# Kernel tuning notes

Measured on AMD Instinct MI355X. Metric: run time of the kernel, lower is better.

The kernel has to match this reference:

```python
import jax, jax.numpy as jnp
import numpy as np

B, L, E, H = 64, 512, 1024, 1024


def setup_inputs() -> dict:
    key = jax.random.key(0)
    ks = jax.random.split(key, 12)
    u = lambda k, s: jax.random.uniform(k, s, jnp.float32, -0.1, 0.1)
    inp = {
        "inputs": jax.random.normal(ks[0], (B, L, E), jnp.float32),
        "input_m": jax.random.randint(ks[1], (B, L), 0, 2).astype(jnp.int32),
    }
    # torch Linear convention: y = x @ W.T + b; biases init to 0 per init_weights()
    for j, n in enumerate(["f", "i", "o", "c"]):
        inp[f"W{n}x"] = u(ks[2 + j], (H, E))
        inp[f"b{n}x"] = jnp.zeros((H,), jnp.float32)
        inp[f"W{n}m"] = u(ks[6 + j], (H, H))
        inp[f"b{n}m"] = jnp.zeros((H,), jnp.float32)
    return inp


def _lstm(inputs, mask_f, Wfx, bfx, Wix, bix, Wox, box, Wcx, bcx,
          Wfm, bfm, Wim, bim, Wom, bom, Wcm, bcm):
    # Fuse the 4 input projections into one GEMM over all timesteps (same math)
    Wx = jnp.concatenate([Wfx, Wix, Wox, Wcx], axis=0)   # [4H, E]
    bx = jnp.concatenate([bfx, bix, box, bcx], axis=0)   # [4H]
    Wm = jnp.concatenate([Wfm, Wim, Wom, Wcm], axis=0)   # [4H, H]
    bm = jnp.concatenate([bfm, bim, bom, bcm], axis=0)   # [4H]

    xproj = jnp.einsum('ble,ge->blg', inputs, Wx) + bx   # [B, L, 4H]
    xs = jnp.moveaxis(xproj, 1, 0)                       # [L, B, 4H]
    ms = mask_f.T[:, :, None]                            # [L, B, 1]

    h0 = jnp.zeros((inputs.shape[0], Wm.shape[1]), inputs.dtype)
    c0 = jnp.zeros_like(h0)

    def step(carry, xm):
        h, c = carry
        xg, m = xm
        g = xg + h @ Wm.T + bm                           # [B, 4H]
        f, i, o, ct = jnp.split(g, 4, axis=-1)
        f = jax.nn.sigmoid(f)
        i = jax.nn.sigmoid(i)
        o = jax.nn.sigmoid(o)
        ct = jnp.tanh(ct)
        c_new = f * c + i * ct                           # cell always updated (as in source)
        hx = o * jnp.tanh(c_new)
        h_new = hx * m + h * (1.0 - m)                   # mask applies to hidden only
        return (h_new, c_new), h_new

    (h_t, c_t), outs = jax.lax.scan(step, (h0, c0), (xs, ms))
    outputs = jnp.moveaxis(outs, 0, 1)                   # [B, L, H]
    return outputs, h_t, c_t


def reference(inputs, input_m, Wfx, bfx, Wix, bix, Wox, box, Wcx, bcx,
              Wfm, bfm, Wim, bim, Wom, bom, Wcm, bcm):
    mask_f = input_m.astype(inputs.dtype)
    return _lstm(inputs, mask_f, Wfx, bfx, Wix, bix, Wox, box, Wcx, bcx,
                 Wfm, bfm, Wim, bim, Wom, bom, Wcm, bcm)
```

## Files before the change

kernel.cpp:

```cpp
#include <hip/hip_runtime.h>


#define B_   64
#define L_   512
#define E_   1024
#define H_   1024

typedef __attribute__((ext_vector_type(8))) short bf16x8;
typedef __attribute__((ext_vector_type(4))) float f32x4;

#define MFMA16(a, b, c) __builtin_amdgcn_mfma_f32_16x16x32_bf16((a), (b), (c), 0, 0, 0)

__device__ __forceinline__ unsigned short f2b(float f) {
  unsigned int u = __float_as_uint(f);
  u += 0x7fffu + ((u >> 16) & 1u);
  return (unsigned short)(u >> 16);
}

__device__ __forceinline__ float sigmoidf_(float x) { return 1.0f / (1.0f + __expf(-x)); }
__device__ __forceinline__ float tanhf_(float x) { return 2.0f / (1.0f + __expf(-2.0f * x)) - 1.0f; }

__global__ __launch_bounds__(256) void pack4(const float* __restrict__ s0, const float* __restrict__ s1,
                                             const float* __restrict__ s2, const float* __restrict__ s3,
                                             unsigned short* __restrict__ dst) {
  int e = (blockIdx.x * 256 + threadIdx.x) * 4;
  int r = e >> 10, col = e & 1023;
  int c = r >> 2, g = r & 3;
  const float* s = g == 0 ? s0 : g == 1 ? s1 : g == 2 ? s2 : s3;
  float4 v = *reinterpret_cast<const float4*>(s + c * 1024 + col);
  ushort4 o;
  o.x = f2b(v.x); o.y = f2b(v.y); o.z = f2b(v.z); o.w = f2b(v.w);
  *reinterpret_cast<ushort4*>(dst + e) = o;
}

__global__ __launch_bounds__(256) void pack_bs(const float* __restrict__ bfx, const float* __restrict__ bix,
                                               const float* __restrict__ box, const float* __restrict__ bcx,
                                               const float* __restrict__ bfm, const float* __restrict__ bim,
                                               const float* __restrict__ bom, const float* __restrict__ bcm,
                                               float* __restrict__ bsum) {
  int i = blockIdx.x * 256 + threadIdx.x;
  int c = i >> 2, g = i & 3;
  const float* px = g == 0 ? bfx : g == 1 ? bix : g == 2 ? box : bcx;
  const float* pm = g == 0 ? bfm : g == 1 ? bim : g == 2 ? bom : bcm;
  bsum[i] = px[c] + pm[c];
}

__global__ __launch_bounds__(256) void zero_state(float* __restrict__ hst, float* __restrict__ cst,
                                                  unsigned short* __restrict__ hbf0) {
  int i = blockIdx.x * 256 + threadIdx.x;
  hst[i] = 0.0f;
  cst[i] = 0.0f;
  hbf0[i] = 0;
}

__global__ __launch_bounds__(256) void gemm_chunk(const float* __restrict__ x,
                                                  const unsigned short* __restrict__ wxp,
                                                  const float* __restrict__ bsum,
                                                  float* __restrict__ xproj,
                                                  int t0, int tshift) {
  __shared__ unsigned short As[128 * 40];
  __shared__ unsigned short Bs[128 * 40];
  const int tid = threadIdx.x;
  const int wave = tid >> 6, lane = tid & 63;
  const int lr = lane & 15, lk = lane >> 4;
  const int mt = blockIdx.x >> 5, nt = blockIdx.x & 31;
  const int m0 = mt * 128, n0 = nt * 128;
  const int wm = (wave >> 1) * 64, wn = (wave & 1) * 64;
  const int Tm1 = (1 << tshift) - 1;

  const int srow = tid >> 1, scol = (tid & 1) * 16;
  const int am = m0 + srow;
  const float* arow = x + ((size_t)(am >> tshift) * 512 + t0 + (am & Tm1)) * 1024 + scol;
  const unsigned short* brow = wxp + (size_t)(n0 + srow) * 1024 + scol;
  unsigned short* asd = As + srow * 40 + scol;
  unsigned short* bsd = Bs + srow * 40 + scol;

  f32x4 acc[4][4] = {};

  for (int k0 = 0; k0 < 1024; k0 += 32) {
    __syncthreads();
    float4 a0 = *reinterpret_cast<const float4*>(arow + k0);
    float4 a1 = *reinterpret_cast<const float4*>(arow + k0 + 4);
    float4 a2 = *reinterpret_cast<const float4*>(arow + k0 + 8);
    float4 a3 = *reinterpret_cast<const float4*>(arow + k0 + 12);
    bf16x8 av0, av1;
    av0[0] = (short)f2b(a0.x); av0[1] = (short)f2b(a0.y); av0[2] = (short)f2b(a0.z); av0[3] = (short)f2b(a0.w);
    av0[4] = (short)f2b(a1.x); av0[5] = (short)f2b(a1.y); av0[6] = (short)f2b(a1.z); av0[7] = (short)f2b(a1.w);
    av1[0] = (short)f2b(a2.x); av1[1] = (short)f2b(a2.y); av1[2] = (short)f2b(a2.z); av1[3] = (short)f2b(a2.w);
    av1[4] = (short)f2b(a3.x); av1[5] = (short)f2b(a3.y); av1[6] = (short)f2b(a3.z); av1[7] = (short)f2b(a3.w);
    *reinterpret_cast<bf16x8*>(asd) = av0;
    *reinterpret_cast<bf16x8*>(asd + 8) = av1;
    *reinterpret_cast<bf16x8*>(bsd) = *reinterpret_cast<const bf16x8*>(brow + k0);
    *reinterpret_cast<bf16x8*>(bsd + 8) = *reinterpret_cast<const bf16x8*>(brow + k0 + 8);
    __syncthreads();

    bf16x8 avf[4], bvf[4];
#pragma unroll
    for (int i = 0; i < 4; ++i)
      avf[i] = *reinterpret_cast<const bf16x8*>(As + (wm + 16 * i + lr) * 40 + lk * 8);
#pragma unroll
    for (int i = 0; i < 4; ++i)
      bvf[i] = *reinterpret_cast<const bf16x8*>(Bs + (wn + 16 * i + lr) * 40 + lk * 8);
#pragma unroll
    for (int mi = 0; mi < 4; ++mi)
#pragma unroll
      for (int ni = 0; ni < 4; ++ni)
        acc[mi][ni] = MFMA16(avf[mi], bvf[ni], acc[mi][ni]);
  }

#pragma unroll
  for (int ni = 0; ni < 4; ++ni) {
    int gn = n0 + wn + 16 * ni + lr;
    float bias = bsum[gn];
#pragma unroll
    for (int mi = 0; mi < 4; ++mi) {
      int gm = m0 + wm + 16 * mi + lk * 4;
#pragma unroll
      for (int j = 0; j < 4; ++j)
        xproj[(size_t)(gm + j) * 4096 + gn] = acc[mi][ni][j] + bias;
    }
  }
}

__global__ __launch_bounds__(512) void lstm_step(const unsigned short* __restrict__ hbf,
                                                 const unsigned short* __restrict__ wmp,
                                                 const float* __restrict__ xproj,
                                                 const int* __restrict__ msk,
                                                 float* __restrict__ hst,
                                                 float* __restrict__ cst,
                                                 unsigned short* __restrict__ hbf_out,
                                                 float* __restrict__ out,
                                                 float* __restrict__ hT,
                                                 float* __restrict__ cT,
                                                 int t, int tl, int T, int last) {
  __shared__ float gsh[8][64][20];
  const int tid = threadIdx.x;
  const int kq = tid >> 6, lane = tid & 63;
  const int lr = lane & 15, lk = lane >> 4;
  const int c0 = blockIdx.x * 4;
  const int r0 = blockIdx.x * 16;

  const int bb = tid >> 2, cc = tid & 3;
  float4 xq;
  float cold = 0.f, hold = 0.f, mval = 0.f;
  int si = 0;
  if (tid < 256) {
    xq = *reinterpret_cast<const float4*>(xproj + ((size_t)bb * T + tl) * 4096 + r0 + cc * 4);
    si = bb * H_ + c0 + cc;
    cold = cst[si];
    hold = hst[si];
    mval = (float)msk[bb * L_ + t];
  }

  const unsigned short* ap = hbf + lr * H_ + kq * 128 + lk * 8;
  const unsigned short* bp = wmp + (size_t)(r0 + lr) * H_ + kq * 128 + lk * 8;

  f32x4 acc[4] = {};
#pragma unroll
  for (int k = 0; k < 128; k += 32) {
    bf16x8 b = *reinterpret_cast<const bf16x8*>(bp + k);
    acc[0] = MFMA16(*reinterpret_cast<const bf16x8*>(ap + k), b, acc[0]);
    acc[1] = MFMA16(*reinterpret_cast<const bf16x8*>(ap + 16 * H_ + k), b, acc[1]);
    acc[2] = MFMA16(*reinterpret_cast<const bf16x8*>(ap + 32 * H_ + k), b, acc[2]);
    acc[3] = MFMA16(*reinterpret_cast<const bf16x8*>(ap + 48 * H_ + k), b, acc[3]);
  }

#pragma unroll
  for (int mi = 0; mi < 4; ++mi)
#pragma unroll
    for (int j = 0; j < 4; ++j)
      gsh[kq][16 * mi + lk * 4 + j][lr] = acc[mi][j];
  __syncthreads();

  if (tid < 256) {
    float vf = xq.x, vi = xq.y, vo = xq.z, vc = xq.w;
#pragma unroll
    for (int q = 0; q < 8; ++q) {
      float4 g4 = *reinterpret_cast<const float4*>(&gsh[q][bb][cc * 4]);
      vf += g4.x; vi += g4.y; vo += g4.z; vc += g4.w;
    }
    float f  = sigmoidf_(vf);
    float i_ = sigmoidf_(vi);
    float o_ = sigmoidf_(vo);
    float ct = tanhf_(vc);

    float cnew = f * cold + i_ * ct;
    cst[si] = cnew;
    float hx = o_ * tanhf_(cnew);
    float hnew = hx * mval + hold * (1.0f - mval);
    hst[si] = hnew;
    hbf_out[si] = f2b(hnew);
    out[((size_t)bb * L_ + t) * H_ + c0 + cc] = hnew;
    if (last) { hT[si] = hnew; cT[si] = cnew; }
  }
}


extern "C" void kernel_launch(void* const* d_in, const int* in_sizes, int n_in,
                              void* d_out, int out_size, void* d_ws, size_t ws_size,
                              hipStream_t stream) {
  (void)in_sizes; (void)n_in; (void)out_size;

  const float* x   = (const float*)d_in[0];
  const int*   msk = (const int*)d_in[1];
  const float* Wfx = (const float*)d_in[2];
  const float* bfx = (const float*)d_in[3];
  const float* Wfm = (const float*)d_in[4];
  const float* bfm = (const float*)d_in[5];
  const float* Wix = (const float*)d_in[6];
  const float* bix = (const float*)d_in[7];
  const float* Wim = (const float*)d_in[8];
  const float* bim = (const float*)d_in[9];
  const float* Wox = (const float*)d_in[10];
  const float* box = (const float*)d_in[11];
  const float* Wom = (const float*)d_in[12];
  const float* bom = (const float*)d_in[13];
  const float* Wcx = (const float*)d_in[14];
  const float* bcx = (const float*)d_in[15];
  const float* Wcm = (const float*)d_in[16];
  const float* bcm = (const float*)d_in[17];

  char* ws = (char*)d_ws;
  unsigned short* wxp  = (unsigned short*)(ws + 0);
  unsigned short* wmp  = (unsigned short*)(ws + 8388608ull);
  float*          bsum = (float*)(ws + 16777216ull);
  float*          hst  = (float*)(ws + 16793600ull);
  float*          cst  = (float*)(ws + 17055744ull);
  unsigned short* hbf0 = (unsigned short*)(ws + 17317888ull);
  unsigned short* hbf1 = (unsigned short*)(ws + 17448960ull);
  float*          xproj = (float*)(ws + 17580032ull);

  int T = 128;
  while (T > 8 && 17580032ull + (size_t)T * 1048576ull > ws_size) T >>= 1;
  int tshift = (T == 128) ? 7 : (T == 64) ? 6 : (T == 32) ? 5 : (T == 16) ? 4 : 3;

  pack4<<<4096, 256, 0, stream>>>(Wfx, Wix, Wox, Wcx, wxp);
  pack4<<<4096, 256, 0, stream>>>(Wfm, Wim, Wom, Wcm, wmp);
  pack_bs<<<16, 256, 0, stream>>>(bfx, bix, box, bcx, bfm, bim, bom, bcm, bsum);
  zero_state<<<256, 256, 0, stream>>>(hst, cst, hbf0);

  float* out = (float*)d_out;
  float* hT = out + (size_t)B_ * L_ * H_;
  float* cT = hT + (size_t)B_ * H_;

  const int nchunks = 512 / T;
  for (int c = 0; c < nchunks; ++c) {
    const int t0 = c * T;
    gemm_chunk<<<(T / 2) * 32, 256, 0, stream>>>(x, wxp, bsum, xproj, t0, tshift);
    for (int tl = 0; tl < T; ++tl) {
      const int t = t0 + tl;
      const unsigned short* hin = (t & 1) ? hbf1 : hbf0;
      unsigned short* hout = (t & 1) ? hbf0 : hbf1;
      lstm_step<<<256, 512, 0, stream>>>(hin, wmp, xproj, msk, hst, cst, hout,
                                         out, hT, cT, t, tl, T, t == L_ - 1);
    }
  }
}
```

Before: 5.825 ms.

## Replace per-timestep LSTM launches with persistent cooperative kernel using grid sync

```diff
diff --git a/kernel.cpp b/kernel.cpp
--- a/kernel.cpp
+++ b/kernel.cpp
@@ -1,4 +1,7 @@
 #include <hip/hip_runtime.h>
+#include <hip/hip_cooperative_groups.h>
+
+namespace cg = cooperative_groups;
 
 
 #define B_   64
@@ -122,17 +125,18 @@
   }
 }
 
-__global__ __launch_bounds__(512) void lstm_step(const unsigned short* __restrict__ hbf,
-                                                 const unsigned short* __restrict__ wmp,
-                                                 const float* __restrict__ xproj,
-                                                 const int* __restrict__ msk,
-                                                 float* __restrict__ hst,
-                                                 float* __restrict__ cst,
-                                                 unsigned short* __restrict__ hbf_out,
-                                                 float* __restrict__ out,
-                                                 float* __restrict__ hT,
-                                                 float* __restrict__ cT,
-                                                 int t, int tl, int T, int last) {
+__global__ __launch_bounds__(512) void lstm_chunk(unsigned short* __restrict__ hbf0,
+                                                  unsigned short* __restrict__ hbf1,
+                                                  const unsigned short* __restrict__ wmp,
+                                                  const float* __restrict__ xproj,
+                                                  const int* __restrict__ msk,
+                                                  float* __restrict__ hst,
+                                                  float* __restrict__ cst,
+                                                  float* __restrict__ out,
+                                                  float* __restrict__ hT,
+                                                  float* __restrict__ cT,
+                                                  int t0, int T, int last_chunk) {
+  cg::grid_group grid = cg::this_grid();
   __shared__ float gsh[8][64][20];
   const int tid = threadIdx.x;
   const int kq = tid >> 6, lane = tid & 63;
@@ -140,58 +144,76 @@
   const int c0 = blockIdx.x * 4;
   const int r0 = blockIdx.x * 16;
 
+  const unsigned short* bp = wmp + (size_t)(r0 + lr) * H_ + kq * 128 + lk * 8;
+  bf16x8 bfr[4];
+#pragma unroll
+  for (int kk = 0; kk < 4; ++kk)
+    bfr[kk] = *reinterpret_cast<const bf16x8*>(bp + kk * 32);
+
   const int bb = tid >> 2, cc = tid & 3;
-  float4 xq;
-  float cold = 0.f, hold = 0.f, mval = 0.f;
-  int si = 0;
+  const int si = bb * H_ + c0 + cc;
+  float c_reg = 0.f, h_reg = 0.f;
+  if (tid < 256) { c_reg = cst[si]; h_reg = hst[si]; }
+
+  const int aoff = lr * H_ + kq * 128 + lk * 8;
+
+  for (int tl = 0; tl < T; ++tl) {
+    const int t = t0 + tl;
+    const unsigned short* hin = (t & 1) ? hbf1 : hbf0;
+    unsigned short* hout = (t & 1) ? hbf0 : hbf1;
+
+    float4 xq = {0.f, 0.f, 0.f, 0.f};
+    float mval = 0.f;
+    if (tid < 256) {
+      xq = *reinterpret_cast<const float4*>(xproj + ((size_t)bb * T + tl) * 4096 + r0 + cc * 4);
+      mval = (float)msk[bb * L_ + t];
+    }
+
+    const unsigned short* ap = hin + aoff;
+    f32x4 acc[4] = {};
+#pragma unroll
+    for (int kk = 0; kk < 4; ++kk) {
+      const int k = kk * 32;
+      acc[0] = MFMA16(*reinterpret_cast<const bf16x8*>(ap + k), bfr[kk], acc[0]);
+      acc[1] = MFMA16(*reinterpret_cast<const bf16x8*>(ap + 16 * H_ + k), bfr[kk], acc[1]);
+      acc[2] = MFMA16(*reinterpret_cast<const bf16x8*>(ap + 32 * H_ + k), bfr[kk], acc[2]);
+      acc[3] = MFMA16(*reinterpret_cast<const bf16x8*>(ap + 48 * H_ + k), bfr[kk], acc[3]);
+    }
+
+#pragma unroll
+    for (int mi = 0; mi < 4; ++mi)
+#pragma unroll
+      for (int j = 0; j < 4; ++j)
+        gsh[kq][16 * mi + lk * 4 + j][lr] = acc[mi][j];
+    __syncthreads();
+
+    if (tid < 256) {
+      float vf = xq.x, vi = xq.y, vo = xq.z, vc = xq.w;
+#pragma unroll
+      for (int q = 0; q < 8; ++q) {
+        float4 g4 = *reinterpret_cast<const float4*>(&gsh[q][bb][cc * 4]);
+        vf += g4.x; vi += g4.y; vo += g4.z; vc += g4.w;
+      }
+      float f  = sigmoidf_(vf);
+      float i_ = sigmoidf_(vi);
+      float o_ = sigmoidf_(vo);
+      float ct = tanhf_(vc);
+
+      float cnew = f * c_reg + i_ * ct;
+      c_reg = cnew;
+      float hx = o_ * tanhf_(cnew);
+      float hnew = hx * mval + h_reg * (1.0f - mval);
+      h_reg = hnew;
+      hout[si] = f2b(hnew);
+      out[((size_t)bb * L_ + t) * H_ + c0 + cc] = hnew;
+    }
+    grid.sync();
+  }
+
   if (tid < 256) {
-    xq = *reinterpret_cast<const float4*>(xproj + ((size_t)bb * T + tl) * 4096 + r0 + cc * 4);
-    si = bb * H_ + c0 + cc;
-    cold = cst[si];
-    hold = hst[si];
-    mval = (float)msk[bb * L_ + t];
-  }
-
-  const unsigned short* ap = hbf + lr * H_ + kq * 128 + lk * 8;
-  const unsigned short* bp = wmp + (size_t)(r0 + lr) * H_ + kq * 128 + lk * 8;
-
-  f32x4 acc[4] = {};
-#pragma unroll
-  for (int k = 0; k < 128; k += 32) {
-    bf16x8 b = *reinterpret_cast<const bf16x8*>(bp + k);
-    acc[0] = MFMA16(*reinterpret_cast<const bf16x8*>(ap + k), b, acc[0]);
-    acc[1] = MFMA16(*reinterpret_cast<const bf16x8*>(ap + 16 * H_ + k), b, acc[1]);
-    acc[2] = MFMA16(*reinterpret_cast<const bf16x8*>(ap + 32 * H_ + k), b, acc[2]);
-    acc[3] = MFMA16(*reinterpret_cast<const bf16x8*>(ap + 48 * H_ + k), b, acc[3]);
-  }
-
-#pragma unroll
-  for (int mi = 0; mi < 4; ++mi)
-#pragma unroll
-    for (int j = 0; j < 4; ++j)
-      gsh[kq][16 * mi + lk * 4 + j][lr] = acc[mi][j];
-  __syncthreads();
-
-  if (tid < 256) {
-    float vf = xq.x, vi = xq.y, vo = xq.z, vc = xq.w;
-#pragma unroll
-    for (int q = 0; q < 8; ++q) {
-      float4 g4 = *reinterpret_cast<const float4*>(&gsh[q][bb][cc * 4]);
-      vf += g4.x; vi += g4.y; vo += g4.z; vc += g4.w;
-    }
-    float f  = sigmoidf_(vf);
-    float i_ = sigmoidf_(vi);
-    float o_ = sigmoidf_(vo);
-    float ct = tanhf_(vc);
-
-    float cnew = f * cold + i_ * ct;
-    cst[si] = cnew;
-    float hx = o_ * tanhf_(cnew);
-    float hnew = hx * mval + hold * (1.0f - mval);
-    hst[si] = hnew;
-    hbf_out[si] = f2b(hnew);
-    out[((size_t)bb * L_ + t) * H_ + c0 + cc] = hnew;
-    if (last) { hT[si] = hnew; cT[si] = cnew; }
+    cst[si] = c_reg;
+    hst[si] = h_reg;
+    if (last_chunk) { hT[si] = h_reg; cT[si] = c_reg; }
   }
 }
 
@@ -245,14 +267,13 @@
 
   const int nchunks = 512 / T;
   for (int c = 0; c < nchunks; ++c) {
-    const int t0 = c * T;
+    int t0 = c * T;
     gemm_chunk<<<(T / 2) * 32, 256, 0, stream>>>(x, wxp, bsum, xproj, t0, tshift);
-    for (int tl = 0; tl < T; ++tl) {
-      const int t = t0 + tl;
-      const unsigned short* hin = (t & 1) ? hbf1 : hbf0;
-      unsigned short* hout = (t & 1) ? hbf0 : hbf1;
-      lstm_step<<<256, 512, 0, stream>>>(hin, wmp, xproj, msk, hst, cst, hout,
-                                         out, hT, cT, t, tl, T, t == L_ - 1);
-    }
-  }
-}
+
+    int lastc = (c == nchunks - 1) ? 1 : 0;
+    void* args[] = {(void*)&hbf0, (void*)&hbf1, (void*)&wmp, (void*)&xproj,
+                    (void*)&msk,  (void*)&hst,  (void*)&cst, (void*)&out,
+                    (void*)&hT,   (void*)&cT,   (void*)&t0,  (void*)&T, (void*)&lastc};
+    hipLaunchCooperativeKernel((void*)lstm_chunk, dim3(256), dim3(512), args, 0, stream);
+  }
+}
```

After: 19.03 ms. 3.27x slower.
